# Performance work log

Measured on AMD Instinct MI355X. Metric: run time of the kernel, lower is better.

Reference implementation:

```python
import jax, jax.numpy as jnp
import numpy as np

# dims
B, S = 1, 32768          # batch, grid seqlen (32^3 latent grid)
NQ, NE = 32768, 262144   # mesh query nodes, grid->query edges
IN, EMB, HID, BOT, PREDH, OUT, NDIM = 192, 192, 192, 192, 192, 4, 3
MAX_WAVELENGTH = 10000.0


def sincos_embed(coords, dim, ndim):
    # ContinuousSincosEmbed: dim % ndim == 0 and (dim//ndim) even here -> no padding
    eff = dim // ndim                                     # 64 dims per coordinate
    omega = 1.0 / MAX_WAVELENGTH ** (jnp.arange(0, eff, 2, dtype=jnp.float32) / eff)  # [eff//2]
    out = coords[..., None] * omega                       # [N, ndim, eff//2]
    emb = jnp.concatenate([jnp.sin(out), jnp.cos(out)], axis=-1)  # [N, ndim, eff]
    return emb.reshape(coords.shape[0], ndim * eff)       # [N, dim]


def _linear_params(key, fan_in, fan_out):
    k1, k2 = jax.random.split(key)
    lim = 1.0 / np.sqrt(fan_in)
    w = jax.random.uniform(k1, (fan_in, fan_out), jnp.float32, -lim, lim)
    b = jax.random.uniform(k2, (fan_out,), jnp.float32, -lim, lim)
    return w, b


def setup_inputs() -> dict:
    key = jax.random.key(0)
    ks = jax.random.split(key, 10)
    x = jax.random.normal(ks[0], (B, S, IN), jnp.float32)
    query_pos = jax.random.uniform(ks[1], (NQ, NDIM), jnp.float32) * 100.0
    # edges sorted by query index (required by the CSR segment reduce in the original)
    qidx = jnp.sort(jax.random.randint(ks[2], (NE,), 0, NQ))
    gidx = jax.random.randint(ks[3], (NE,), 0, B * S)
    grid_to_query_edges = jnp.stack([qidx, gidx], axis=1).astype(jnp.int64)
    proj_w, proj_b = _linear_params(ks[4], IN, EMB)
    msg0_w, msg0_b = _linear_params(ks[5], 2 * EMB, 2 * HID)
    msg1_w, msg1_b = _linear_params(ks[6], 2 * HID, 2 * HID)
    msg2_w, msg2_b = _linear_params(ks[7], 2 * HID, BOT)
    pred0_w, pred0_b = _linear_params(ks[8], BOT, PREDH)
    pred1_w, pred1_b = _linear_params(ks[9], PREDH, OUT)
    return dict(x=x, query_pos=query_pos, grid_to_query_edges=grid_to_query_edges,
                proj_w=proj_w, proj_b=proj_b,
                msg0_w=msg0_w, msg0_b=msg0_b, msg1_w=msg1_w, msg1_b=msg1_b,
                msg2_w=msg2_w, msg2_b=msg2_b,
                pred0_w=pred0_w, pred0_b=pred0_b, pred1_w=pred1_w, pred1_b=pred1_b)


def reference(x, query_pos, grid_to_query_edges,
              proj_w, proj_b, msg0_w, msg0_b, msg1_w, msg1_b, msg2_w, msg2_b,
              pred0_w, pred0_b, pred1_w, pred1_b):
    gelu = lambda t: jax.nn.gelu(t, approximate=False)  # torch nn.GELU default (erf)
    # flatten grid tokens and project
    xf = x.reshape(-1, x.shape[-1]) @ proj_w + proj_b          # [B*S, EMB]
    qe = sincos_embed(query_pos, EMB, NDIM)                    # [NQ, EMB]
    qidx = grid_to_query_edges[:, 0]
    gidx = grid_to_query_edges[:, 1]
    # gather + concat per edge
    h = jnp.concatenate([xf[gidx], qe[qidx]], axis=1)          # [NE, 2*EMB]
    # message MLP
    h = gelu(h @ msg0_w + msg0_b)
    h = gelu(h @ msg1_w + msg1_b)
    h = h @ msg2_w + msg2_b                                    # [NE, BOT]
    # segment mean to query nodes (empty segments -> 0, matching segment_csr mean)
    nq = query_pos.shape[0]
    seg_sum = jax.ops.segment_sum(h, qidx, num_segments=nq)    # [NQ, BOT]
    cnt = jax.ops.segment_sum(jnp.ones((qidx.shape[0], 1), h.dtype), qidx, num_segments=nq)
    m = seg_sum / jnp.maximum(cnt, 1.0)
    # prediction head
    out = gelu(m @ pred0_w + pred0_b) @ pred1_w + pred1_b      # [NQ, OUT]
    return out
```

## Files before the change

### kernel.cpp

```cpp
#include <hip/hip_runtime.h>
#include <math.h>

#define N_Q    32768
#define N_E    262144

typedef _Float16 half8 __attribute__((ext_vector_type(8)));
typedef _Float16 half4v __attribute__((ext_vector_type(4)));
typedef float f32x4 __attribute__((ext_vector_type(4)));

__device__ __forceinline__ float gelu_f(float x) {
    float ax = fabsf(x);
    float t = __builtin_amdgcn_rcpf(fmaf(0.33269070724668f, ax, 1.0f));
    float poly = t * fmaf(t, fmaf(t, 0.7478556f, -0.0958798f), 0.3480242f);
    float e = exp2f(-0.72134752044448f * ax * ax);
    float u = fmaf(-poly, e, 1.0f);
    return 0.5f * fmaf(ax, u, x);
}

__device__ __forceinline__ void pack_one(const float* __restrict__ W,
                                         _Float16* __restrict__ Wp,
                                         int K, int N, int blk0, int tid) {
    int u = blk0 * 256 + tid;
    if (u * 8 >= K * N) return;
    int l = u & 63, blk = u >> 6;
    int nks = K >> 5;
    int ntile = blk / nks, ks = blk - ntile * nks;
    int n = ntile * 16 + (l & 15);
    int k0 = ks * 32 + (l >> 4) * 8;
    half8 v;
    #pragma unroll
    for (int j = 0; j < 8; ++j) v[j] = (_Float16)W[(size_t)(k0 + j) * N + n];
    *(half8*)(Wp + (size_t)u * 8) = v;
}

__global__ __launch_bounds__(256, 4) void preppack_kernel(
    const float* __restrict__ proj_w, const float* __restrict__ proj_b,
    const float* __restrict__ msg0_w, const float* __restrict__ msg0_b,
    const float* __restrict__ msg1_w, const float* __restrict__ msg2_w,
    const float* __restrict__ pred0_w,
    _Float16* __restrict__ WpC, float* __restrict__ bc,
    _Float16* __restrict__ WpQ, _Float16* __restrict__ Wp1,
    _Float16* __restrict__ Wp2, _Float16* __restrict__ WpH)
{
    int b = blockIdx.x, t = threadIdx.x;
    if (b < 290) {
        int gid = b * 256 + t;
        if (gid < 73728) {
            int j = gid / 384, n = gid - j * 384;
            float a = 0.0f;
            for (int k = 0; k < 192; ++k)
                a = fmaf(proj_w[j * 192 + k], msg0_w[k * 384 + n], a);
            int off = (((n >> 4) * 6 + (j >> 5)) * 512) +
                      ((((j >> 3) & 3) * 16 + (n & 15)) * 8) + (j & 7);
            WpC[off] = (_Float16)a;
        } else if (gid < 73728 + 384) {
            int n = gid - 73728;
            float a = msg0_b[n];
            for (int k = 0; k < 192; ++k)
                a = fmaf(proj_b[k], msg0_w[k * 384 + n], a);
            bc[n] = a;
        }
    } else {
        int p = b - 290;
        if      (p < 36)  pack_one(msg0_w + 73728, WpQ, 192, 384, p,       t);
        else if (p < 108) pack_one(msg1_w,         Wp1, 384, 384, p - 36,  t);
        else if (p < 144) pack_one(msg2_w,         Wp2, 384, 192, p - 108, t);
        else              pack_one(pred0_w,        WpH, 192, 192, p - 144, t);
    }
}

#define PK 200

__global__ __launch_bounds__(256, 4) void pgpq_kernel(
    const float* __restrict__ x, const float* __restrict__ qpos,
    const _Float16* __restrict__ WpC, const _Float16* __restrict__ WpQ,
    const float* __restrict__ bc,
    _Float16* __restrict__ pg, _Float16* __restrict__ pq)
{
    __shared__ _Float16 hA[32 * PK];
    const int t = threadIdx.x;
    const bool isPg = blockIdx.x < 1024;
    const int r0 = (isPg ? blockIdx.x : blockIdx.x - 1024) * 32;
    const int lane = t & 63;
    const int w = t >> 6;
    const int ln = lane & 15, lq = lane >> 4;

    if (isPg) {
        #pragma unroll
        for (int i = 0; i < 6; ++i) {
            int idx = t + 256 * i;
            int r = idx / 48, c4 = idx - r * 48;
            float4 v = ((const float4*)(x + (size_t)(r0 + r) * 192))[c4];
            half4v hv; hv[0] = (_Float16)v.x; hv[1] = (_Float16)v.y;
            hv[2] = (_Float16)v.z; hv[3] = (_Float16)v.w;
            *(half4v*)(hA + r * PK + c4 * 4) = hv;
        }
    } else {
        #pragma unroll
        for (int it = 0; it < 12; ++it) {
            int g2 = t + 256 * it;
            int r = g2 / 96, rem = g2 - r * 96;
            int d = rem >> 5, i = rem & 31;
            float omega = exp2f(-(float)i * 0.41524101186092029f);
            float arg = qpos[(size_t)(r0 + r) * 3 + d] * omega;
            float rev = arg * 0.15915494309189535f;
            rev = rev - floorf(rev);
            hA[r * PK + d * 64 + i]      = (_Float16)__builtin_amdgcn_sinf(rev);
            hA[r * PK + d * 64 + 32 + i] = (_Float16)__builtin_amdgcn_cosf(rev);
        }
    }
    __syncthreads();

    const _Float16* __restrict__ Wp = isPg ? WpC : WpQ;
    _Float16* __restrict__ out = isPg ? pg : pq;

    f32x4 acc[2][6];
    #pragma unroll
    for (int nt = 0; nt < 6; ++nt) {
        f32x4 bv = isPg ? *(const f32x4*)(bc + w * 96 + nt * 16 + lq * 4)
                        : (f32x4){0.f, 0.f, 0.f, 0.f};
        #pragma unroll
        for (int mt = 0; mt < 2; ++mt) acc[mt][nt] = bv;
    }
    #pragma unroll 2
    for (int ks = 0; ks < 6; ++ks) {
        half8 a[2], bf[6];
        #pragma unroll
        for (int mt = 0; mt < 2; ++mt)
            a[mt] = *(const half8*)(hA + (mt * 16 + ln) * PK + ks * 32 + lq * 8);
        #pragma unroll
        for (int nt = 0; nt < 6; ++nt)
            bf[nt] = *(const half8*)(Wp + (size_t)(((w * 6 + nt) * 6 + ks) * 512 + lane * 8));
        #pragma unroll
        for (int nt = 0; nt < 6; ++nt)
            #pragma unroll
            for (int mt = 0; mt < 2; ++mt)
                acc[mt][nt] = __builtin_amdgcn_mfma_f32_16x16x32_f16(bf[nt], a[mt], acc[mt][nt], 0, 0, 0);
    }
    #pragma unroll
    for (int mt = 0; mt < 2; ++mt)
        #pragma unroll
        for (int nt = 0; nt < 6; ++nt) {
            half4v hv;
            #pragma unroll
            for (int r = 0; r < 4; ++r) hv[r] = (_Float16)acc[mt][nt][r];
            *(half4v*)(out + (size_t)(r0 + mt * 16 + ln) * 384 + w * 96 + nt * 16 + lq * 4) = hv;
        }
}

#define PADK 392
#define H2S  196

__global__ __launch_bounds__(512, 6) void edge_mlp_kernel(
    const _Float16* __restrict__ pg, const _Float16* __restrict__ pq,
    const int* __restrict__ edges,
    const _Float16* __restrict__ Wp1, const float* __restrict__ b1,
    const _Float16* __restrict__ Wp2, const float* __restrict__ b2,
    float* __restrict__ seg, float* __restrict__ cnt)
{
    __shared__ _Float16 hA[64 * PADK];
    __shared__ int qi[64];
    float* h2 = (float*)hA;

    const int t = threadIdx.x;
    const int e0 = blockIdx.x * 64;
    const int lane = t & 63;
    const int w = t >> 6;
    const int ln = lane & 15;
    const int lq = lane >> 4;

    if (t < 64) qi[t] = edges[2 * (e0 + t)];

    {
        const int m = t >> 3;
        const int cl = t & 7;
        int2 eg = ((const int2*)edges)[e0 + m];
        const half8* gsrc = (const half8*)(pg + (size_t)eg.y * 384) + cl;
        const half8* qsrc = (const half8*)(pq + (size_t)eg.x * 384) + cl;
        half8* dst = (half8*)(hA + m * PADK + cl * 8);
        #pragma unroll
        for (int i = 0; i < 6; ++i) {
            half8 va = gsrc[i * 8];
            half8 vb = qsrc[i * 8];
            half8 o;
            #pragma unroll
            for (int j = 0; j < 8; ++j)
                o[j] = (_Float16)gelu_f((float)va[j] + (float)vb[j]);
            dst[i * 8] = o;
        }
    }
    __syncthreads();

    {
        f32x4 acc[4][3];
        #pragma unroll
        for (int nt = 0; nt < 3; ++nt) {
            f32x4 bv = *(const f32x4*)(b1 + w * 48 + nt * 16 + lq * 4);
            #pragma unroll
            for (int mt = 0; mt < 4; ++mt) acc[mt][nt] = bv;
        }
        #pragma unroll 2
        for (int ks = 0; ks < 12; ++ks) {
            half8 a[4], bf[3];
            #pragma unroll
            for (int mt = 0; mt < 4; ++mt)
                a[mt] = *(const half8*)(hA + (mt * 16 + ln) * PADK + ks * 32 + lq * 8);
            #pragma unroll
            for (int nt = 0; nt < 3; ++nt)
                bf[nt] = *(const half8*)(Wp1 + (size_t)(((w * 3 + nt) * 12 + ks) * 512 + lane * 8));
            #pragma unroll
            for (int nt = 0; nt < 3; ++nt)
                #pragma unroll
                for (int mt = 0; mt < 4; ++mt)
                    acc[mt][nt] = __builtin_amdgcn_mfma_f32_16x16x32_f16(bf[nt], a[mt], acc[mt][nt], 0, 0, 0);
        }
        __syncthreads();
        #pragma unroll
        for (int mt = 0; mt < 4; ++mt)
            #pragma unroll
            for (int nt = 0; nt < 3; ++nt) {
                half4v hv;
                #pragma unroll
                for (int r = 0; r < 4; ++r) hv[r] = (_Float16)gelu_f(acc[mt][nt][r]);
                *(half4v*)(hA + (mt * 16 + ln) * PADK + w * 48 + nt * 16 + lq * 4) = hv;
            }
        __syncthreads();
    }

    {
        const int n0 = (w & 3) * 48;
        const int mh = (w >> 2) * 2;
        f32x4 acc[2][3];
        #pragma unroll
        for (int nt = 0; nt < 3; ++nt) {
            f32x4 bv = *(const f32x4*)(b2 + n0 + nt * 16 + lq * 4);
            #pragma unroll
            for (int mt = 0; mt < 2; ++mt) acc[mt][nt] = bv;
        }
        #pragma unroll 2
        for (int ks = 0; ks < 12; ++ks) {
            half8 a[2], bf[3];
            #pragma unroll
            for (int mt = 0; mt < 2; ++mt)
                a[mt] = *(const half8*)(hA + ((mh + mt) * 16 + ln) * PADK + ks * 32 + lq * 8);
            #pragma unroll
            for (int nt = 0; nt < 3; ++nt)
                bf[nt] = *(const half8*)(Wp2 + (size_t)((((w & 3) * 3 + nt) * 12 + ks) * 512 + lane * 8));
            #pragma unroll
            for (int nt = 0; nt < 3; ++nt)
                #pragma unroll
                for (int mt = 0; mt < 2; ++mt)
                    acc[mt][nt] = __builtin_amdgcn_mfma_f32_16x16x32_f16(bf[nt], a[mt], acc[mt][nt], 0, 0, 0);
        }
        __syncthreads();
        #pragma unroll
        for (int mt = 0; mt < 2; ++mt)
            #pragma unroll
            for (int nt = 0; nt < 3; ++nt)
                *(f32x4*)(h2 + ((mh + mt) * 16 + ln) * H2S + n0 + nt * 16 + lq * 4) = acc[mt][nt];
        __syncthreads();
    }

    if (t < 192) {
        int half_ = t / 96;
        int cp = t - half_ * 96;
        int col = cp * 2;
        int mlo = half_ * 32, mhi = mlo + 32;
        float ax = 0.0f, ay = 0.0f;
        for (int m = mlo; m < mhi; ++m) {
            float2 v = *(const float2*)(h2 + m * H2S + col);
            ax += v.x; ay += v.y;
            if (m == mhi - 1 || qi[m + 1] != qi[m]) {
                atomicAdd(&seg[(size_t)qi[m] * 192 + col], ax);
                atomicAdd(&seg[(size_t)qi[m] * 192 + col + 1], ay);
                ax = 0.0f; ay = 0.0f;
            }
        }
    } else if (t >= 384 && t < 386) {
        int half_ = t - 384;
        int mlo = half_ * 32, mhi = mlo + 32;
        float run = 1.0f;
        for (int m = mlo + 1; m < mhi; ++m) {
            if (qi[m] != qi[m - 1]) { atomicAdd(&cnt[qi[m - 1]], run); run = 1.0f; }
            else run += 1.0f;
        }
        atomicAdd(&cnt[qi[mhi - 1]], run);
    }
}

#define PSK 196

__global__ __launch_bounds__(256, 3) void head_kernel(
    const float* __restrict__ seg, const float* __restrict__ cnt,
    const _Float16* __restrict__ Wp0, const float* __restrict__ b0,
    const float* __restrict__ w1, const float* __restrict__ b1,
    float* __restrict__ out)
{
    __shared__ _Float16 hA[32 * PK];
    __shared__ float ps[32 * PSK];
    __shared__ float w1s[192 * 4];
    __shared__ float invc[32];
    const int t = threadIdx.x;
    const int r0 = blockIdx.x * 32;
    const int lane = t & 63;
    const int w = t >> 6;
    const int ln = lane & 15, lq = lane >> 4;

    if (t < 32) invc[t] = 1.0f / fmaxf(cnt[r0 + t], 1.0f);
    if (t < 192) ((float4*)w1s)[t] = ((const float4*)w1)[t];
    __syncthreads();

    #pragma unroll
    for (int i = 0; i < 6; ++i) {
        int idx = t + 256 * i;
        int r = idx / 48, c4 = idx - r * 48;
        float inv = invc[r];
        float4 v = ((const float4*)(seg + (size_t)(r0 + r) * 192))[c4];
        half4v hv; hv[0] = (_Float16)(v.x * inv); hv[1] = (_Float16)(v.y * inv);
        hv[2] = (_Float16)(v.z * inv); hv[3] = (_Float16)(v.w * inv);
        *(half4v*)(hA + r * PK + c4 * 4) = hv;
    }
    __syncthreads();

    f32x4 acc[2][3];
    #pragma unroll
    for (int nt = 0; nt < 3; ++nt) {
        f32x4 bv = *(const f32x4*)(b0 + w * 48 + nt * 16 + lq * 4);
        #pragma unroll
        for (int mt = 0; mt < 2; ++mt) acc[mt][nt] = bv;
    }
    #pragma unroll 2
    for (int ks = 0; ks < 6; ++ks) {
        half8 a[2], bf[3];
        #pragma unroll
        for (int mt = 0; mt < 2; ++mt)
            a[mt] = *(const half8*)(hA + (mt * 16 + ln) * PK + ks * 32 + lq * 8);
        #pragma unroll
        for (int nt = 0; nt < 3; ++nt)
            bf[nt] = *(const half8*)(Wp0 + (size_t)(((w * 3 + nt) * 6 + ks) * 512 + lane * 8));
        #pragma unroll
        for (int nt = 0; nt < 3; ++nt)
            #pragma unroll
            for (int mt = 0; mt < 2; ++mt)
                acc[mt][nt] = __builtin_amdgcn_mfma_f32_16x16x32_f16(bf[nt], a[mt], acc[mt][nt], 0, 0, 0);
    }
    #pragma unroll
    for (int mt = 0; mt < 2; ++mt)
        #pragma unroll
        for (int nt = 0; nt < 3; ++nt) {
            f32x4 g;
            #pragma unroll
            for (int r = 0; r < 4; ++r) g[r] = gelu_f(acc[mt][nt][r]);
            *(f32x4*)(ps + (mt * 16 + ln) * PSK + w * 48 + nt * 16 + lq * 4) = g;
        }
    __syncthreads();

    if (t < 128) {
        int r = t >> 2, oo = t & 3;
        float a = b1[oo];
        for (int k = 0; k < 192; ++k)
            a = fmaf(ps[r * PSK + k], w1s[k * 4 + oo], a);
        out[(size_t)(r0 + r) * 4 + oo] = a;
    }
}

extern "C" void kernel_launch(void* const* d_in, const int* in_sizes, int n_in,
                              void* d_out, int out_size, void* d_ws, size_t ws_size,
                              hipStream_t stream) {
    (void)in_sizes; (void)n_in; (void)out_size; (void)ws_size;
    const float* x       = (const float*)d_in[0];
    const float* qpos    = (const float*)d_in[1];
    const int*   edges   = (const int*)d_in[2];
    const float* proj_w  = (const float*)d_in[3];
    const float* proj_b  = (const float*)d_in[4];
    const float* msg0_w  = (const float*)d_in[5];
    const float* msg0_b  = (const float*)d_in[6];
    const float* msg1_w  = (const float*)d_in[7];
    const float* msg1_b  = (const float*)d_in[8];
    const float* msg2_w  = (const float*)d_in[9];
    const float* msg2_b  = (const float*)d_in[10];
    const float* pred0_w = (const float*)d_in[11];
    const float* pred0_b = (const float*)d_in[12];
    const float* pred1_w = (const float*)d_in[13];
    const float* pred1_b = (const float*)d_in[14];
    float* out = (float*)d_out;

    char* ws = (char*)d_ws;
    _Float16* pg  = (_Float16*)(ws);
    _Float16* pq  = (_Float16*)(ws + 25165824);
    float*    seg = (float*)(ws + 50331648);
    float*    cnt = (float*)(ws + 75497472);
    float*    bc  = (float*)(ws + 75628544);
    _Float16* WpC = (_Float16*)(ws + 75630080);
    _Float16* WpQ = (_Float16*)(ws + 75777536);
    _Float16* Wp1 = (_Float16*)(ws + 75924992);
    _Float16* Wp2 = (_Float16*)(ws + 76219904);
    _Float16* WpH = (_Float16*)(ws + 76367360);

    hipMemsetAsync(seg, 0, 25165824 + 131072, stream);
    preppack_kernel<<<452, 256, 0, stream>>>(proj_w, proj_b, msg0_w, msg0_b,
                                             msg1_w, msg2_w, pred0_w,
                                             WpC, bc, WpQ, Wp1, Wp2, WpH);
    pgpq_kernel<<<2048, 256, 0, stream>>>(x, qpos, WpC, WpQ, bc, pg, pq);
    edge_mlp_kernel<<<4096, 512, 0, stream>>>(pg, pq, edges,
                                              Wp1, msg1_b, Wp2, msg2_b,
                                              seg, cnt);
    head_kernel<<<1024, 256, 0, stream>>>(seg, cnt, WpH, pred0_b,
                                          pred1_w, pred1_b, out);
}
```

Baseline: 351.1 us.

## Use 32x32x16 MFMA for msg1 layer, fold seg memset into pgpq, widen atomics

The msg1 GEMM in the edge MLP switches from 16x16x32 MFMA tiles to 32x32x16 tiles, with a matching new weight packing layout. Each wave now computes a 32-row by 96-column block, so fewer A-fragment LDS reads are needed per MFMA. The zeroing of the segment-sum buffer moves from a separate memset into extra blocks of the pgpq kernel. The segment atomic reduction uses 384 threads with one column each instead of 192 threads with two. The changes touch packing, GEMM layout and launch structure together.

```diff
diff --git a/kernel.cpp b/kernel.cpp
--- a/kernel.cpp
+++ b/kernel.cpp
@@ -7,6 +7,7 @@
 typedef _Float16 half8 __attribute__((ext_vector_type(8)));
 typedef _Float16 half4v __attribute__((ext_vector_type(4)));
 typedef float f32x4 __attribute__((ext_vector_type(4)));
+typedef float f32x16 __attribute__((ext_vector_type(16)));
 
 __device__ __forceinline__ float gelu_f(float x) {
     float ax = fabsf(x);
@@ -27,6 +28,22 @@
     int ntile = blk / nks, ks = blk - ntile * nks;
     int n = ntile * 16 + (l & 15);
     int k0 = ks * 32 + (l >> 4) * 8;
+    half8 v;
+    #pragma unroll
+    for (int j = 0; j < 8; ++j) v[j] = (_Float16)W[(size_t)(k0 + j) * N + n];
+    *(half8*)(Wp + (size_t)u * 8) = v;
+}
+
+__device__ __forceinline__ void pack32_one(const float* __restrict__ W,
+                                           _Float16* __restrict__ Wp,
+                                           int K, int N, int blk0, int tid) {
+    int u = blk0 * 256 + tid;
+    if (u * 8 >= K * N) return;
+    int l = u & 63, blk = u >> 6;
+    int nks = K >> 4;
+    int ntile = blk / nks, ks = blk - ntile * nks;
+    int n = ntile * 32 + (l & 31);
+    int k0 = ks * 16 + (l >> 5) * 8;
     half8 v;
     #pragma unroll
     for (int j = 0; j < 8; ++j) v[j] = (_Float16)W[(size_t)(k0 + j) * N + n];
@@ -62,10 +79,10 @@
         }
     } else {
         int p = b - 290;
-        if      (p < 36)  pack_one(msg0_w + 73728, WpQ, 192, 384, p,       t);
-        else if (p < 108) pack_one(msg1_w,         Wp1, 384, 384, p - 36,  t);
-        else if (p < 144) pack_one(msg2_w,         Wp2, 384, 192, p - 108, t);
-        else              pack_one(pred0_w,        WpH, 192, 192, p - 144, t);
+        if      (p < 36)  pack_one  (msg0_w + 73728, WpQ, 192, 384, p,       t);
+        else if (p < 108) pack32_one(msg1_w,         Wp1, 384, 384, p - 36,  t);
+        else if (p < 144) pack_one  (msg2_w,         Wp2, 384, 192, p - 108, t);
+        else              pack_one  (pred0_w,        WpH, 192, 192, p - 144, t);
     }
 }
 
@@ -75,10 +92,19 @@
     const float* __restrict__ x, const float* __restrict__ qpos,
     const _Float16* __restrict__ WpC, const _Float16* __restrict__ WpQ,
     const float* __restrict__ bc,
-    _Float16* __restrict__ pg, _Float16* __restrict__ pq)
+    _Float16* __restrict__ pg, _Float16* __restrict__ pq,
+    float* __restrict__ seg)
 {
     __shared__ _Float16 hA[32 * PK];
     const int t = threadIdx.x;
+
+    if (blockIdx.x >= 2048) {
+        float4* dst = (float4*)seg + (size_t)(blockIdx.x - 2048) * 4096 + t;
+        #pragma unroll
+        for (int i = 0; i < 16; ++i) dst[i * 256] = (float4){0.f, 0.f, 0.f, 0.f};
+        return;
+    }
+
     const bool isPg = blockIdx.x < 1024;
     const int r0 = (isPg ? blockIdx.x : blockIdx.x - 1024) * 32;
     const int lane = t & 63;
@@ -192,37 +218,38 @@
     __syncthreads();
 
     {
-        f32x4 acc[4][3];
-        #pragma unroll
-        for (int nt = 0; nt < 3; ++nt) {
-            f32x4 bv = *(const f32x4*)(b1 + w * 48 + nt * 16 + lq * 4);
-            #pragma unroll
-            for (int mt = 0; mt < 4; ++mt) acc[mt][nt] = bv;
-        }
-        #pragma unroll 2
-        for (int ks = 0; ks < 12; ++ks) {
-            half8 a[4], bf[3];
-            #pragma unroll
-            for (int mt = 0; mt < 4; ++mt)
-                a[mt] = *(const half8*)(hA + (mt * 16 + ln) * PADK + ks * 32 + lq * 8);
+        const int wm = w >> 2, wn = w & 3;
+        const int l31 = lane & 31, lh = lane >> 5;
+        const int cb = wn * 96;
+        f32x16 acc[3];
+        #pragma unroll
+        for (int nt = 0; nt < 3; ++nt)
+            #pragma unroll
+            for (int g = 0; g < 4; ++g) {
+                float4 bv = *(const float4*)(b1 + cb + nt * 32 + g * 8 + lh * 4);
+                acc[nt][4 * g + 0] = bv.x; acc[nt][4 * g + 1] = bv.y;
+                acc[nt][4 * g + 2] = bv.z; acc[nt][4 * g + 3] = bv.w;
+            }
+        #pragma unroll 4
+        for (int ks = 0; ks < 24; ++ks) {
+            half8 a = *(const half8*)(hA + (wm * 32 + l31) * PADK + ks * 16 + lh * 8);
+            half8 bf[3];
             #pragma unroll
             for (int nt = 0; nt < 3; ++nt)
-                bf[nt] = *(const half8*)(Wp1 + (size_t)(((w * 3 + nt) * 12 + ks) * 512 + lane * 8));
+                bf[nt] = *(const half8*)(Wp1 + (size_t)(((wn * 3 + nt) * 24 + ks) * 512 + lane * 8));
             #pragma unroll
             for (int nt = 0; nt < 3; ++nt)
-                #pragma unroll
-                for (int mt = 0; mt < 4; ++mt)
-                    acc[mt][nt] = __builtin_amdgcn_mfma_f32_16x16x32_f16(bf[nt], a[mt], acc[mt][nt], 0, 0, 0);
+                acc[nt] = __builtin_amdgcn_mfma_f32_32x32x16_f16(bf[nt], a, acc[nt], 0, 0, 0);
         }
         __syncthreads();
         #pragma unroll
-        for (int mt = 0; mt < 4; ++mt)
-            #pragma unroll
-            for (int nt = 0; nt < 3; ++nt) {
+        for (int nt = 0; nt < 3; ++nt)
+            #pragma unroll
+            for (int g = 0; g < 4; ++g) {
                 half4v hv;
                 #pragma unroll
-                for (int r = 0; r < 4; ++r) hv[r] = (_Float16)gelu_f(acc[mt][nt][r]);
-                *(half4v*)(hA + (mt * 16 + ln) * PADK + w * 48 + nt * 16 + lq * 4) = hv;
+                for (int q = 0; q < 4; ++q) hv[q] = (_Float16)gelu_f(acc[nt][4 * g + q]);
+                *(half4v*)(hA + (wm * 32 + l31) * PADK + cb + nt * 32 + g * 8 + lh * 4) = hv;
             }
         __syncthreads();
     }
@@ -261,22 +288,19 @@
         __syncthreads();
     }
 
-    if (t < 192) {
-        int half_ = t / 96;
-        int cp = t - half_ * 96;
-        int col = cp * 2;
+    if (t < 384) {
+        int half_ = t >= 192;
+        int col = t - half_ * 192;
         int mlo = half_ * 32, mhi = mlo + 32;
-        float ax = 0.0f, ay = 0.0f;
+        float a = 0.0f;
         for (int m = mlo; m < mhi; ++m) {
-            float2 v = *(const float2*)(h2 + m * H2S + col);
-            ax += v.x; ay += v.y;
+            a += h2[m * H2S + col];
             if (m == mhi - 1 || qi[m + 1] != qi[m]) {
-                atomicAdd(&seg[(size_t)qi[m] * 192 + col], ax);
-                atomicAdd(&seg[(size_t)qi[m] * 192 + col + 1], ay);
-                ax = 0.0f; ay = 0.0f;
+                atomicAdd(&seg[(size_t)qi[m] * 192 + col], a);
+                a = 0.0f;
             }
         }
-    } else if (t >= 384 && t < 386) {
+    } else if (t < 386) {
         int half_ = t - 384;
         int mlo = half_ * 32, mhi = mlo + 32;
         float run = 1.0f;
@@ -397,11 +421,10 @@
     _Float16* Wp2 = (_Float16*)(ws + 76219904);
     _Float16* WpH = (_Float16*)(ws + 76367360);
 
-    hipMemsetAsync(seg, 0, 25165824 + 131072, stream);
     preppack_kernel<<<452, 256, 0, stream>>>(proj_w, proj_b, msg0_w, msg0_b,
                                              msg1_w, msg2_w, pred0_w,
                                              WpC, bc, WpQ, Wp1, Wp2, WpH);
-    pgpq_kernel<<<2048, 256, 0, stream>>>(x, qpos, WpC, WpQ, bc, pg, pq);
+    pgpq_kernel<<<2434, 256, 0, stream>>>(x, qpos, WpC, WpQ, bc, pg, pq, seg);
     edge_mlp_kernel<<<4096, 512, 0, stream>>>(pg, pq, edges,
                                               Wp1, msg1_b, Wp2, msg2_b,
                                               seg, cnt);
```

Result: no change. 352.1 us (+0.3%).
